# Kernel optimization log

Hardware: AMD Instinct MI355X
Metric: run time of the kernel (lower is better)

## Reference

```python
import jax, jax.numpy as jnp
import numpy as np

H = 64  # hidden size


def _gru_cell(x, h, Wih, Whh, bih, bhh):
    """PyTorch-convention GRU cell. x:[B,in], h:[B,H]. Gate order: r, z, n."""
    gi = x @ Wih.T + bih              # [B, 3H]
    gh = h @ Whh.T + bhh              # [B, 3H]
    ir, iz, in_ = jnp.split(gi, 3, axis=-1)
    hr, hz, hn = jnp.split(gh, 3, axis=-1)
    r = jax.nn.sigmoid(ir + hr)
    z = jax.nn.sigmoid(iz + hz)
    n = jnp.tanh(in_ + r * hn)
    return (1.0 - z) * n + z * h


def setup_inputs() -> dict:
    key = jax.random.key(0)
    B, T, NIN = 4096, 256, 6
    ks = jax.random.split(key, 24)

    def w(k, shape, fan):
        return (jax.random.normal(k, shape, jnp.float32) / np.sqrt(fan).astype(np.float32))

    inp = {"x": jax.random.normal(ks[0], (B, T, NIN), jnp.float32)}
    # encoder layer 0 (input 6) and layer 1 (input 64)
    inp["enc_Wih0"] = w(ks[1], (3 * H, NIN), H)
    inp["enc_Whh0"] = w(ks[2], (3 * H, H), H)
    inp["enc_bih0"] = w(ks[3], (3 * H,), H)
    inp["enc_bhh0"] = w(ks[4], (3 * H,), H)
    inp["enc_Wih1"] = w(ks[5], (3 * H, H), H)
    inp["enc_Whh1"] = w(ks[6], (3 * H, H), H)
    inp["enc_bih1"] = w(ks[7], (3 * H,), H)
    inp["enc_bhh1"] = w(ks[8], (3 * H,), H)
    # decoder layer 0 (input 1) and layer 1 (input 64)
    inp["dec_Wih0"] = w(ks[9], (3 * H, 1), H)
    inp["dec_Whh0"] = w(ks[10], (3 * H, H), H)
    inp["dec_bih0"] = w(ks[11], (3 * H,), H)
    inp["dec_bhh0"] = w(ks[12], (3 * H,), H)
    inp["dec_Wih1"] = w(ks[13], (3 * H, H), H)
    inp["dec_Whh1"] = w(ks[14], (3 * H, H), H)
    inp["dec_bih1"] = w(ks[15], (3 * H,), H)
    inp["dec_bhh1"] = w(ks[16], (3 * H,), H)
    # output head
    inp["out_W"] = w(ks[17], (1, H), H)
    inp["out_b"] = w(ks[18], (1,), H)
    inp["target_len"] = 180
    return inp


def reference(x, enc_Wih0, enc_Whh0, enc_bih0, enc_bhh0,
              enc_Wih1, enc_Whh1, enc_bih1, enc_bhh1,
              dec_Wih0, dec_Whh0, dec_bih0, dec_bhh0,
              dec_Wih1, dec_Whh1, dec_bih1, dec_bhh1,
              out_W, out_b, target_len):
    B = x.shape[0]
    dtype = x.dtype

    # ---- encoder: 2-layer GRU over x, return final hidden per layer ----
    seq = jnp.swapaxes(x, 0, 1)  # [T, B, 6] time-major
    enc_layers = [(enc_Wih0, enc_Whh0, enc_bih0, enc_bhh0),
                  (enc_Wih1, enc_Whh1, enc_bih1, enc_bhh1)]
    h_finals = []
    for (Wih, Whh, bih, bhh) in enc_layers:
        def step(h, xt, Wih=Wih, Whh=Whh, bih=bih, bhh=bhh):
            hn = _gru_cell(xt, h, Wih, Whh, bih, bhh)
            return hn, hn
        h_last, seq = jax.lax.scan(step, jnp.zeros((B, H), dtype), seq)
        h_finals.append(h_last)

    def dec_step(carry, _):
        h0, h1, prev = carry
        h0 = _gru_cell(prev, h0, dec_Wih0, dec_Whh0, dec_bih0, dec_bhh0)
        h1 = _gru_cell(h0, h1, dec_Wih1, dec_Whh1, dec_bih1, dec_bhh1)
        cv = h1 @ out_W.T + out_b  # [B, 1]
        return (h0, h1, cv), cv

    prev0 = jnp.zeros((B, 1), dtype)
    _, outs = jax.lax.scan(dec_step, (h_finals[0], h_finals[1], prev0),
                           None, length=target_len)
    return jnp.swapaxes(outs, 0, 1)  # [B, target_len, 1]
```

## Files before the change

### kernel.cpp

```cpp
#include <hip/hip_runtime.h>
#include <cstdint>

typedef _Float16 half8 __attribute__((ext_vector_type(8)));
typedef __attribute__((ext_vector_type(4))) float floatx4;

#define TSEQ 256
#define TDEC 180
#define NIN  6
#define GROWS 16
#define NBLK (4096 / GROWS)
#define NSL 4
#define RS0 104
#define RS1 72
#define L2E 1.4426950408889634f

__device__ __forceinline__ floatx4 mfma16(half8 a, half8 b, floatx4 c) {
  return __builtin_amdgcn_mfma_f32_16x16x32_f16(a, b, c, 0, 0, 0);
}

__device__ __forceinline__ float sigm2(float v) {
  return __builtin_amdgcn_rcpf(1.0f + __builtin_amdgcn_exp2f(-v));
}
__device__ __forceinline__ float tanh2(float v) {
  return fmaf(2.0f, __builtin_amdgcn_rcpf(1.0f + __builtin_amdgcn_exp2f(-v)), -1.0f);
}

__device__ __forceinline__ half8 ldh8(const _Float16* p) { return *(const half8*)p; }

#define PASS2_I3(F0, F1, r, z, g, W, QR, QZ, QG) do {                   \
  r = mfma16(F0, W[0][0], QR); z = mfma16(F0, W[1][0], QZ); g = mfma16(F0, W[2][0], QG); \
  r = mfma16(F1, W[0][1], r);  z = mfma16(F1, W[1][1], z);  g = mfma16(F1, W[2][1], g);  \
} while (0)

#define PASS2_A2I1(F0, F1, r, z, g, W, QG) do {                         \
  r = mfma16(F0, W[0][0], r); z = mfma16(F0, W[1][0], z); g = mfma16(F0, W[2][0], QG); \
  r = mfma16(F1, W[0][1], r); z = mfma16(F1, W[1][1], z); g = mfma16(F1, W[2][1], g);  \
} while (0)

#define PASS1_A2I1(F0, r, z, g, W, QG) do {                             \
  r = mfma16(F0, W[0][0], r); z = mfma16(F0, W[1][0], z); g = mfma16(F0, W[2][0], QG); \
} while (0)

#define SYNC() do {                                         \
  asm volatile("s_waitcnt lgkmcnt(0)" ::: "memory");        \
  __builtin_amdgcn_s_barrier();                             \
  asm volatile("" ::: "memory");                            \
} while (0)

__global__ void __launch_bounds__(512, 2)
gru_persist(const float* __restrict__ x,
            const float* __restrict__ eWih0, const float* __restrict__ eWhh0,
            const float* __restrict__ ebih0, const float* __restrict__ ebhh0,
            const float* __restrict__ eWih1, const float* __restrict__ eWhh1,
            const float* __restrict__ ebih1, const float* __restrict__ ebhh1,
            const float* __restrict__ dWih0, const float* __restrict__ dWhh0,
            const float* __restrict__ dbih0, const float* __restrict__ dbhh0,
            const float* __restrict__ dWih1, const float* __restrict__ dWhh1,
            const float* __restrict__ dbih1, const float* __restrict__ dbhh1,
            const float* __restrict__ outW, const float* __restrict__ outB,
            float* __restrict__ out)
{
  __shared__ __align__(16) _Float16 s0[NSL][16][RS0];
  __shared__ __align__(16) _Float16 s1[NSL][16][RS1];

  const int tid  = threadIdx.x;
  const bool isA = tid < 256;
  const int wvL  = (tid >> 6) & 3;
  const int lane = tid & 63;
  const int c    = lane & 15;
  const int q    = lane >> 4;
  const int u    = wvL * 16 + c;
  const long base = (long)blockIdx.x * GROWS;

  for (int i = tid; i < NSL * 16 * RS0; i += 512) ((uint16_t*)s0)[i] = 0;
  for (int i = tid; i < NSL * 16 * RS1; i += 512) ((uint16_t*)s1)[i] = 0;
  if (tid < GROWS * NIN) {
    int m = tid / 6, i2 = tid - m * 6;
    s0[0][m][64 + i2] = (_Float16)x[(base + m) * (TSEQ * NIN) + i2];
  }

  half8 W1[3][2], W2[3][2];
  half8 W1d[3][2], W2d[3][2];
  float hr[4] = {0, 0, 0, 0};
  const float SC[3] = {L2E, L2E, 2.0f * L2E};

  auto loadW64 = [&](const float* W, half8 (&D)[3][2]) {
    #pragma unroll
    for (int s = 0; s < 3; s++) {
      const int n = (s * 4 + wvL) * 16 + c;
      #pragma unroll
      for (int kt = 0; kt < 2; kt++) {
        const int k0 = kt * 32 + q * 8;
        #pragma unroll
        for (int j = 0; j < 8; j++) D[s][kt][j] = (_Float16)(SC[s] * W[n * 64 + k0 + j]);
      }
    }
  };

  const float ob = outB[0];
  float cR, cZ, c3, c4;
  float dR, dZ, d3, d4;
  float bR0 = 0, bZ0 = 0, b30 = 0, b40 = 0;
  float wk[2][8];
  if (isA) {
    loadW64(eWhh0, W1);
    #pragma unroll
    for (int s = 0; s < 3; s++) {
      const int n = (s * 4 + wvL) * 16 + c;
      #pragma unroll
      for (int kt = 0; kt < 2; kt++)
        #pragma unroll
        for (int j = 0; j < 8; j++) {
          float v = (kt == 0 && q == 0 && j < NIN) ? SC[s] * eWih0[n * NIN + j] : 0.0f;
          W2[s][kt][j] = (_Float16)v;
        }
    }
    loadW64(dWhh0, W1d);
    #pragma unroll
    for (int s = 0; s < 3; s++) {
      const int n = (s * 4 + wvL) * 16 + c;
      const float wd = SC[s] * dWih0[n];
      #pragma unroll
      for (int kt = 0; kt < 2; kt++) {
        const int k0 = kt * 32 + q * 8;
        #pragma unroll
        for (int j = 0; j < 8; j++) W2d[s][kt][j] = (_Float16)(wd * outW[k0 + j]);
      }
    }
    cR = L2E * (ebih0[u] + ebhh0[u]);
    cZ = L2E * (ebih0[64 + u] + ebhh0[64 + u]);
    c3 = 2.0f * L2E * ebhh0[128 + u];
    c4 = 2.0f * L2E * ebih0[128 + u];
    bR0 = L2E * (dbih0[u] + dbhh0[u]);
    bZ0 = L2E * (dbih0[64 + u] + dbhh0[64 + u]);
    b30 = 2.0f * L2E * dbhh0[128 + u];
    b40 = 2.0f * L2E * dbih0[128 + u];
    dR = bR0 + L2E * (dWih0[u] * ob);
    dZ = bZ0 + L2E * (dWih0[64 + u] * ob);
    d3 = b30;
    d4 = b40 + 2.0f * L2E * (dWih0[128 + u] * ob);
  } else {
    loadW64(eWih1, W1); loadW64(eWhh1, W2);
    loadW64(dWih1, W1d); loadW64(dWhh1, W2d);
    cR = L2E * (ebih1[u] + ebhh1[u]);
    cZ = L2E * (ebih1[64 + u] + ebhh1[64 + u]);
    c3 = 2.0f * L2E * ebih1[128 + u];
    c4 = 2.0f * L2E * ebhh1[128 + u];
    dR = L2E * (dbih1[u] + dbhh1[u]);
    dZ = L2E * (dbih1[64 + u] + dbhh1[64 + u]);
    d3 = 2.0f * L2E * dbih1[128 + u];
    d4 = 2.0f * L2E * dbhh1[128 + u];
    #pragma unroll
    for (int kt = 0; kt < 2; kt++)
      #pragma unroll
      for (int j = 0; j < 8; j++) wk[kt][j] = outW[kt * 32 + q * 8 + j];
  }
  __syncthreads();

  if (isA) {
    floatx4 QR = {cR, cR, cR, cR}, QZ = {cZ, cZ, cZ, cZ};
    floatx4 Q3 = {c3, c3, c3, c3}, Q4 = {c4, c4, c4, c4};
    const bool doX = (wvL == 0) && (lane < 48);
    const float *px0 = nullptr, *px1 = nullptr;
    int xo0 = 0, xo1 = 0;
    float xa0 = 0.f, xa1 = 0.f, xb0 = 0.f, xb1 = 0.f;
    if (doX) {
      int s0_ = lane, s1_ = lane + 48;
      int m0 = s0_ / 6, i0 = s0_ - m0 * 6, m1 = s1_ / 6, i1 = s1_ - m1 * 6;
      px0 = x + (base + m0) * (TSEQ * NIN) + i0;
      px1 = x + (base + m1) * (TSEQ * NIN) + i1;
      xo0 = m0 * RS0 + 64 + i0; xo1 = m1 * RS0 + 64 + i1;
      xa0 = px0[NIN];     xa1 = px1[NIN];
      xb0 = px0[2 * NIN]; xb1 = px1[2 * NIN];
    }
    for (int k = 0; k < TSEQ; k += 4) {
      #pragma unroll
      for (int h4 = 0; h4 < 4; h4++) {
        const int i_ = k + h4, p = h4, pn = (h4 + 1) & 3;
        const half8 a0 = ldh8(&s0[p][c][q * 8]);
        const half8 a1 = ldh8(&s0[p][c][32 + q * 8]);
        const half8 xf = ldh8(&s0[p][c][64 + q * 8]);
        floatx4 aR, aZ, a3, a4;
        PASS2_I3(a0, a1, aR, aZ, a3, W1, QR, QZ, Q3);
        PASS1_A2I1(xf, aR, aZ, a4, W2, Q4);
        if (doX && i_ + 1 < TSEQ) {
          ((_Float16*)s0[pn])[xo0] = (_Float16)xa0;
          ((_Float16*)s0[pn])[xo1] = (_Float16)xa1;
          xa0 = xb0; xa1 = xb1;
          if (i_ + 3 < TSEQ) { xb0 = px0[(i_ + 3) * NIN]; xb1 = px1[(i_ + 3) * NIN]; }
        }
        #pragma unroll
        for (int r4 = 0; r4 < 4; r4++) {
          const float gr = sigm2(aR[r4]);
          const float gz = sigm2(aZ[r4]);
          const float nn = tanh2(a4[r4] + gr * a3[r4]);
          const float hn = nn + gz * (hr[r4] - nn);
          hr[r4] = hn;
          s0[pn][q * 4 + r4][u] = (_Float16)hn;
        }
        SYNC();
      }
    }
    {
      const half8 a0 = ldh8(&s0[0][c][q * 8]);
      const half8 a1 = ldh8(&s0[0][c][32 + q * 8]);
      const floatx4 TR = {bR0, bR0, bR0, bR0}, TZ = {bZ0, bZ0, bZ0, bZ0};
      const floatx4 T3 = {b30, b30, b30, b30};
      floatx4 aR, aZ, a3;
      floatx4 a4 = {b40, b40, b40, b40};
      PASS2_I3(a0, a1, aR, aZ, a3, W1d, TR, TZ, T3);
      #pragma unroll
      for (int r4 = 0; r4 < 4; r4++) {
        const float gr = sigm2(aR[r4]);
        const float gz = sigm2(aZ[r4]);
        const float nn = tanh2(a4[r4] + gr * a3[r4]);
        const float hn = nn + gz * (hr[r4] - nn);
        hr[r4] = hn;
        s0[1][q * 4 + r4][u] = (_Float16)hn;
      }
      SYNC();
    }
    QR = (floatx4){dR, dR, dR, dR}; QZ = (floatx4){dZ, dZ, dZ, dZ};
    Q3 = (floatx4){d3, d3, d3, d3}; Q4 = (floatx4){d4, d4, d4, d4};
    for (int i_ = TSEQ + 1; i_ < TSEQ + TDEC; i_++) {
      const int p = i_ & 3, pn = (i_ + 1) & 3;
      const half8 a0 = ldh8(&s0[p][c][q * 8]);
      const half8 a1 = ldh8(&s0[p][c][32 + q * 8]);
      floatx4 aR, aZ, a3, a4;
      PASS2_I3(a0, a1, aR, aZ, a3, W1d, QR, QZ, Q3);
      SYNC();
      const half8 b0 = ldh8(&s1[p][c][q * 8]);
      const half8 b1 = ldh8(&s1[p][c][32 + q * 8]);
      PASS2_A2I1(b0, b1, aR, aZ, a4, W2d, Q4);
      #pragma unroll
      for (int r4 = 0; r4 < 4; r4++) {
        const float gr = sigm2(aR[r4]);
        const float gz = sigm2(aZ[r4]);
        const float nn = tanh2(a4[r4] + gr * a3[r4]);
        const float hn = nn + gz * (hr[r4] - nn);
        hr[r4] = hn;
        s0[pn][q * 4 + r4][u] = (_Float16)hn;
      }
      SYNC();
    }
    SYNC();
  } else {
    floatx4 QR = {cR, cR, cR, cR}, QZ = {cZ, cZ, cZ, cZ};
    floatx4 Q3 = {c3, c3, c3, c3}, Q4 = {c4, c4, c4, c4};
    for (int k = 0; k < TSEQ; k += 4) {
      #pragma unroll
      for (int h4 = 0; h4 < 4; h4++) {
        const int kk = k + h4;
        if (kk > 0) {
          const int p = (h4 + 3) & 3, pn = h4;
          const half8 f0 = ldh8(&s1[p][c][q * 8]);
          const half8 f1 = ldh8(&s1[p][c][32 + q * 8]);
          floatx4 aR, aZ, a3, a4;
          PASS2_I3(f0, f1, aR, aZ, a4, W2, QR, QZ, Q4);
          const half8 g0 = ldh8(&s0[pn][c][q * 8]);
          const half8 g1 = ldh8(&s0[pn][c][32 + q * 8]);
          PASS2_A2I1(g0, g1, aR, aZ, a3, W1, Q3);
          #pragma unroll
          for (int r4 = 0; r4 < 4; r4++) {
            const float gr = sigm2(aR[r4]);
            const float gz = sigm2(aZ[r4]);
            const float nn = tanh2(a3[r4] + gr * a4[r4]);
            const float hn = nn + gz * (hr[r4] - nn);
            hr[r4] = hn;
            s1[pn][q * 4 + r4][u] = (_Float16)hn;
          }
        }
        SYNC();
      }
    }
    {
      const half8 f0 = ldh8(&s1[3][c][q * 8]);
      const half8 f1 = ldh8(&s1[3][c][32 + q * 8]);
      floatx4 aR, aZ, a3, a4;
      PASS2_I3(f0, f1, aR, aZ, a4, W2, QR, QZ, Q4);
      const half8 g0 = ldh8(&s0[0][c][q * 8]);
      const half8 g1 = ldh8(&s0[0][c][32 + q * 8]);
      PASS2_A2I1(g0, g1, aR, aZ, a3, W1, Q3);
      #pragma unroll
      for (int r4 = 0; r4 < 4; r4++) {
        const float gr = sigm2(aR[r4]);
        const float gz = sigm2(aZ[r4]);
        const float nn = tanh2(a3[r4] + gr * a4[r4]);
        const float hn = nn + gz * (hr[r4] - nn);
        hr[r4] = hn;
        s1[0][q * 4 + r4][u] = (_Float16)hn;
      }
      SYNC();
    }
    QR = (floatx4){dR, dR, dR, dR}; QZ = (floatx4){dZ, dZ, dZ, dZ};
    Q3 = (floatx4){d3, d3, d3, d3}; Q4 = (floatx4){d4, d4, d4, d4};
    {
      const half8 f0 = ldh8(&s1[0][c][q * 8]);
      const half8 f1 = ldh8(&s1[0][c][32 + q * 8]);
      floatx4 aR, aZ, a3, a4;
      PASS2_I3(f0, f1, aR, aZ, a4, W2d, QR, QZ, Q4);
      const half8 g0 = ldh8(&s0[1][c][q * 8]);
      const half8 g1 = ldh8(&s0[1][c][32 + q * 8]);
      PASS2_A2I1(g0, g1, aR, aZ, a3, W1d, Q3);
      #pragma unroll
      for (int r4 = 0; r4 < 4; r4++) {
        const float gr = sigm2(aR[r4]);
        const float gz = sigm2(aZ[r4]);
        const float nn = tanh2(a3[r4] + gr * a4[r4]);
        const float hn = nn + gz * (hr[r4] - nn);
        hr[r4] = hn;
        s1[1][q * 4 + r4][u] = (_Float16)hn;
      }
      SYNC();
    }
    for (int i_ = TSEQ + 1; i_ < TSEQ + TDEC; i_++) {
      const int p = i_ & 3, pn = (i_ + 1) & 3;
      const half8 f0 = ldh8(&s1[p][c][q * 8]);
      const half8 f1 = ldh8(&s1[p][c][32 + q * 8]);
      floatx4 aR, aZ, a3, a4;
      PASS2_I3(f0, f1, aR, aZ, a4, W2d, QR, QZ, Q4);
      if (wvL == 0) {
        float cv = 0.0f;
        #pragma unroll
        for (int j = 0; j < 8; j++) {
          cv = fmaf((float)f0[j], wk[0][j], cv);
          cv = fmaf((float)f1[j], wk[1][j], cv);
        }
        cv += __shfl_xor(cv, 16);
        cv += __shfl_xor(cv, 32);
        if (lane < 16) out[(base + lane) * TDEC + (i_ - TSEQ - 1)] = cv + ob;
      }
      SYNC();
      const half8 g0 = ldh8(&s0[pn][c][q * 8]);
      const half8 g1 = ldh8(&s0[pn][c][32 + q * 8]);
      PASS2_A2I1(g0, g1, aR, aZ, a3, W1d, Q3);
      #pragma unroll
      for (int r4 = 0; r4 < 4; r4++) {
        const float gr = sigm2(aR[r4]);
        const float gz = sigm2(aZ[r4]);
        const float nn = tanh2(a3[r4] + gr * a4[r4]);
        const float hn = nn + gz * (hr[r4] - nn);
        hr[r4] = hn;
        s1[pn][q * 4 + r4][u] = (_Float16)hn;
      }
      SYNC();
    }
    if (wvL == 0) {
      const half8 f0 = ldh8(&s1[0][c][q * 8]);
      const half8 f1 = ldh8(&s1[0][c][32 + q * 8]);
      float cv = 0.0f;
      #pragma unroll
      for (int j = 0; j < 8; j++) {
        cv = fmaf((float)f0[j], wk[0][j], cv);
        cv = fmaf((float)f1[j], wk[1][j], cv);
      }
      cv += __shfl_xor(cv, 16);
      cv += __shfl_xor(cv, 32);
      if (lane < 16) out[(base + lane) * TDEC + (TDEC - 1)] = cv + ob;
    }
  }
}

extern "C" void kernel_launch(void* const* d_in, const int* in_sizes, int n_in,
                              void* d_out, int out_size, void* d_ws, size_t ws_size,
                              hipStream_t stream) {
  (void)in_sizes; (void)n_in; (void)d_ws; (void)ws_size; (void)out_size;
  const float* x     = (const float*)d_in[0];
  const float* eWih0 = (const float*)d_in[1];
  const float* eWhh0 = (const float*)d_in[2];
  const float* ebih0 = (const float*)d_in[3];
  const float* ebhh0 = (const float*)d_in[4];
  const float* eWih1 = (const float*)d_in[5];
  const float* eWhh1 = (const float*)d_in[6];
  const float* ebih1 = (const float*)d_in[7];
  const float* ebhh1 = (const float*)d_in[8];
  const float* dWih0 = (const float*)d_in[9];
  const float* dWhh0 = (const float*)d_in[10];
  const float* dbih0 = (const float*)d_in[11];
  const float* dbhh0 = (const float*)d_in[12];
  const float* dWih1 = (const float*)d_in[13];
  const float* dWhh1 = (const float*)d_in[14];
  const float* dbih1 = (const float*)d_in[15];
  const float* dbhh1 = (const float*)d_in[16];
  const float* outW  = (const float*)d_in[17];
  const float* outB  = (const float*)d_in[18];
  hipLaunchKernelGGL(gru_persist, dim3(NBLK), dim3(512), 0, stream,
                     x, eWih0, eWhh0, ebih0, ebhh0, eWih1, eWhh1, ebih1, ebhh1,
                     dWih0, dWhh0, dbih0, dbhh0, dWih1, dWhh1, dbih1, dbhh1,
                     outW, outB, (float*)d_out);
}
```

Baseline: 360.6 us.

## Split GRU step into gate and nonlinearity phases with extra barriers for overlap

Restructures the warp-specialised layer-0 and layer-1 recurrences so each step's matmul gate phase and nonlinearity phase are separated by a barrier. The other wave group's work can then interleave at finer granularity: layer 1's gate MFMAs overlap layer 0's nonlinearity, and the decoder prefetches the next step's layer-0 gates. This doubles the number of block barriers per timestep to shorten the critical path between the two specialised roles. The barrier counts on the two sides must stay matched exactly, which makes it fragile.

Result: slower. 391.1 us (+8.5%).

```diff
diff --git a/kernel.cpp b/kernel.cpp
--- a/kernel.cpp
+++ b/kernel.cpp
@@ -183,6 +183,7 @@
         floatx4 aR, aZ, a3, a4;
         PASS2_I3(a0, a1, aR, aZ, a3, W1, QR, QZ, Q3);
         PASS1_A2I1(xf, aR, aZ, a4, W2, Q4);
+        SYNC();
         if (doX && i_ + 1 < TSEQ) {
           ((_Float16*)s0[pn])[xo0] = (_Float16)xa0;
           ((_Float16*)s0[pn])[xo1] = (_Float16)xa1;
@@ -207,8 +208,9 @@
       const floatx4 TR = {bR0, bR0, bR0, bR0}, TZ = {bZ0, bZ0, bZ0, bZ0};
       const floatx4 T3 = {b30, b30, b30, b30};
       floatx4 aR, aZ, a3;
+      PASS2_I3(a0, a1, aR, aZ, a3, W1d, TR, TZ, T3);
+      SYNC();
       floatx4 a4 = {b40, b40, b40, b40};
-      PASS2_I3(a0, a1, aR, aZ, a3, W1d, TR, TZ, T3);
       #pragma unroll
       for (int r4 = 0; r4 < 4; r4++) {
         const float gr = sigm2(aR[r4]);
@@ -220,17 +222,21 @@
       }
       SYNC();
     }
+    SYNC();
     QR = (floatx4){dR, dR, dR, dR}; QZ = (floatx4){dZ, dZ, dZ, dZ};
     Q3 = (floatx4){d3, d3, d3, d3}; Q4 = (floatx4){d4, d4, d4, d4};
+    floatx4 aR, aZ, a3;
+    {
+      const half8 a0 = ldh8(&s0[1][c][q * 8]);
+      const half8 a1 = ldh8(&s0[1][c][32 + q * 8]);
+      PASS2_I3(a0, a1, aR, aZ, a3, W1d, QR, QZ, Q3);
+      SYNC();
+    }
     for (int i_ = TSEQ + 1; i_ < TSEQ + TDEC; i_++) {
       const int p = i_ & 3, pn = (i_ + 1) & 3;
-      const half8 a0 = ldh8(&s0[p][c][q * 8]);
-      const half8 a1 = ldh8(&s0[p][c][32 + q * 8]);
-      floatx4 aR, aZ, a3, a4;
-      PASS2_I3(a0, a1, aR, aZ, a3, W1d, QR, QZ, Q3);
-      SYNC();
       const half8 b0 = ldh8(&s1[p][c][q * 8]);
       const half8 b1 = ldh8(&s1[p][c][32 + q * 8]);
+      floatx4 a4;
       PASS2_A2I1(b0, b1, aR, aZ, a4, W2d, Q4);
       #pragma unroll
       for (int r4 = 0; r4 < 4; r4++) {
@@ -242,62 +248,57 @@
         s0[pn][q * 4 + r4][u] = (_Float16)hn;
       }
       SYNC();
-    }
-    SYNC();
+      if (i_ + 1 < TSEQ + TDEC) {
+        const half8 a0 = ldh8(&s0[pn][c][q * 8]);
+        const half8 a1 = ldh8(&s0[pn][c][32 + q * 8]);
+        PASS2_I3(a0, a1, aR, aZ, a3, W1d, QR, QZ, Q3);
+      }
+      SYNC();
+    }
   } else {
     floatx4 QR = {cR, cR, cR, cR}, QZ = {cZ, cZ, cZ, cZ};
     floatx4 Q3 = {c3, c3, c3, c3}, Q4 = {c4, c4, c4, c4};
-    for (int k = 0; k < TSEQ; k += 4) {
-      #pragma unroll
-      for (int h4 = 0; h4 < 4; h4++) {
-        const int kk = k + h4;
-        if (kk > 0) {
-          const int p = (h4 + 3) & 3, pn = h4;
-          const half8 f0 = ldh8(&s1[p][c][q * 8]);
-          const half8 f1 = ldh8(&s1[p][c][32 + q * 8]);
-          floatx4 aR, aZ, a3, a4;
-          PASS2_I3(f0, f1, aR, aZ, a4, W2, QR, QZ, Q4);
-          const half8 g0 = ldh8(&s0[pn][c][q * 8]);
-          const half8 g1 = ldh8(&s0[pn][c][32 + q * 8]);
-          PASS2_A2I1(g0, g1, aR, aZ, a3, W1, Q3);
-          #pragma unroll
-          for (int r4 = 0; r4 < 4; r4++) {
-            const float gr = sigm2(aR[r4]);
-            const float gz = sigm2(aZ[r4]);
-            const float nn = tanh2(a3[r4] + gr * a4[r4]);
-            const float hn = nn + gz * (hr[r4] - nn);
-            hr[r4] = hn;
-            s1[pn][q * 4 + r4][u] = (_Float16)hn;
-          }
-        }
-        SYNC();
-      }
-    }
-    {
-      const half8 f0 = ldh8(&s1[3][c][q * 8]);
-      const half8 f1 = ldh8(&s1[3][c][32 + q * 8]);
-      floatx4 aR, aZ, a3, a4;
-      PASS2_I3(f0, f1, aR, aZ, a4, W2, QR, QZ, Q4);
-      const half8 g0 = ldh8(&s0[0][c][q * 8]);
-      const half8 g1 = ldh8(&s0[0][c][32 + q * 8]);
-      PASS2_A2I1(g0, g1, aR, aZ, a3, W1, Q3);
-      #pragma unroll
-      for (int r4 = 0; r4 < 4; r4++) {
-        const float gr = sigm2(aR[r4]);
-        const float gz = sigm2(aZ[r4]);
-        const float nn = tanh2(a3[r4] + gr * a4[r4]);
-        const float hn = nn + gz * (hr[r4] - nn);
-        hr[r4] = hn;
-        s1[0][q * 4 + r4][u] = (_Float16)hn;
-      }
-      SYNC();
-    }
+    floatx4 aR, aZ, a3, a4;
+
+    #define B_GATES(rs1, rs0) do {                                        \
+      const half8 f0 = ldh8(&s1[rs1][c][q * 8]);                          \
+      const half8 f1 = ldh8(&s1[rs1][c][32 + q * 8]);                     \
+      PASS2_I3(f0, f1, aR, aZ, a4, W2, QR, QZ, Q4);    \
+      const half8 g0 = ldh8(&s0[rs0][c][q * 8]);                          \
+      const half8 g1 = ldh8(&s0[rs0][c][32 + q * 8]);                     \
+      PASS2_A2I1(g0, g1, aR, aZ, a3, W1, Q3);          \
+    } while (0)
+    #define B_NONLIN(ws) do {                                             \
+      _Pragma("unroll")                                                   \
+      for (int r4 = 0; r4 < 4; r4++) {                                    \
+        const float gr = sigm2(aR[r4]);                                   \
+        const float gz = sigm2(aZ[r4]);                                   \
+        const float nn = tanh2(a3[r4] + gr * a4[r4]);                     \
+        const float hn = nn + gz * (hr[r4] - nn);                         \
+        hr[r4] = hn;                                                      \
+        s1[ws][q * 4 + r4][u] = (_Float16)hn;                             \
+      }                                                                   \
+    } while (0)
+
+    SYNC(); SYNC();
+    SYNC();
+    B_GATES(0, 1);
+    SYNC();
+    for (int kk = 0; kk < 63; kk++) {
+      B_NONLIN(1); SYNC(); B_GATES(1, 2); SYNC();
+      B_NONLIN(2); SYNC(); B_GATES(2, 3); SYNC();
+      B_NONLIN(3); SYNC(); B_GATES(3, 0); SYNC();
+      B_NONLIN(0); SYNC(); B_GATES(0, 1); SYNC();
+    }
+    B_NONLIN(1); SYNC(); B_GATES(1, 2); SYNC();
+    B_NONLIN(2); SYNC(); B_GATES(2, 3); SYNC();
+    B_NONLIN(3); SYNC(); B_GATES(3, 0); SYNC();
+    B_NONLIN(0); SYNC();
     QR = (floatx4){dR, dR, dR, dR}; QZ = (floatx4){dZ, dZ, dZ, dZ};
     Q3 = (floatx4){d3, d3, d3, d3}; Q4 = (floatx4){d4, d4, d4, d4};
     {
       const half8 f0 = ldh8(&s1[0][c][q * 8]);
       const half8 f1 = ldh8(&s1[0][c][32 + q * 8]);
-      floatx4 aR, aZ, a3, a4;
       PASS2_I3(f0, f1, aR, aZ, a4, W2d, QR, QZ, Q4);
       const half8 g0 = ldh8(&s0[1][c][q * 8]);
       const half8 g1 = ldh8(&s0[1][c][32 + q * 8]);
@@ -317,8 +318,8 @@
       const int p = i_ & 3, pn = (i_ + 1) & 3;
       const half8 f0 = ldh8(&s1[p][c][q * 8]);
       const half8 f1 = ldh8(&s1[p][c][32 + q * 8]);
-      floatx4 aR, aZ, a3, a4;
-      PASS2_I3(f0, f1, aR, aZ, a4, W2d, QR, QZ, Q4);
+      floatx4 bR, bZ, b3, b4;
+      PASS2_I3(f0, f1, bR, bZ, b4, W2d, QR, QZ, Q4);
       if (wvL == 0) {
         float cv = 0.0f;
         #pragma unroll
@@ -333,12 +334,12 @@
       SYNC();
       const half8 g0 = ldh8(&s0[pn][c][q * 8]);
       const half8 g1 = ldh8(&s0[pn][c][32 + q * 8]);
-      PASS2_A2I1(g0, g1, aR, aZ, a3, W1d, Q3);
+      PASS2_A2I1(g0, g1, bR, bZ, b3, W1d, Q3);
       #pragma unroll
       for (int r4 = 0; r4 < 4; r4++) {
-        const float gr = sigm2(aR[r4]);
-        const float gz = sigm2(aZ[r4]);
-        const float nn = tanh2(a3[r4] + gr * a4[r4]);
+        const float gr = sigm2(bR[r4]);
+        const float gz = sigm2(bZ[r4]);
+        const float nn = tanh2(b3[r4] + gr * b4[r4]);
         const float hn = nn + gz * (hr[r4] - nn);
         hr[r4] = hn;
         s1[pn][q * 4 + r4][u] = (_Float16)hn;
@@ -358,6 +359,8 @@
       cv += __shfl_xor(cv, 32);
       if (lane < 16) out[(base + lane) * TDEC + (TDEC - 1)] = cv + ob;
     }
+    #undef B_GATES
+    #undef B_NONLIN
   }
 }
 
```
